# Performance work log

Hardware: AMD Instinct MI355X
Metric: run time of the kernel (lower is better)

The kernel has to match this reference:

```python
import jax, jax.numpy as jnp
import numpy as np

N_MODES = 3
NEG_SLOPE = 0.2


def setup_inputs() -> dict:
    key = jax.random.key(0)
    k1, k2, k3 = jax.random.split(key, 3)
    T, BN, C = 32, 16384, 128
    h = jax.random.normal(k1, (T, BN, C), dtype=jnp.float32)
    # FNO-style init scale 1/(in*out)
    scale = 1.0 / (C * C)
    w_real = scale * jax.random.normal(k2, (C, C, N_MODES), dtype=jnp.float32)
    w_imag = scale * jax.random.normal(k3, (C, C, N_MODES), dtype=jnp.float32)
    return {"h": h, "w_real": w_real, "w_imag": w_imag}


def reference(h, w_real, w_imag):
    T, BN, C = h.shape
    # (T, BN, C) -> (BN, C, T)
    x = jnp.transpose(h, (1, 2, 0))
    x_ft = jnp.fft.rfft(x, axis=-1)              # (BN, C, T//2+1) complex
    w = w_real + 1j * w_imag                     # (C_in, C_out, modes)
    # mix channels on the lowest n_modes frequencies
    out_low = jnp.einsum("bim,iom->bom", x_ft[..., :N_MODES], w)
    out_ft = jnp.zeros((BN, C, T // 2 + 1), dtype=x_ft.dtype)
    out_ft = out_ft.at[..., :N_MODES].set(out_low)
    y = jnp.fft.irfft(out_ft, n=T, axis=-1)      # (BN, C, T) real
    y = jnp.transpose(y, (2, 0, 1))              # back to (T, BN, C)
    return h + jnp.where(y >= 0, y, NEG_SLOPE * y)
```

## Files before the change

### kernel.cpp

```cpp
#include <hip/hip_runtime.h>
#include <hip/hip_bf16.h>


#define T 32
#define BN 16384
#define C 128
#define NBC (BN * C)

typedef __attribute__((ext_vector_type(4))) float f32x4;
typedef __attribute__((ext_vector_type(8))) short bf16x8;
typedef __attribute__((ext_vector_type(4))) unsigned short u16x4;

__constant__ float COS32[32] = {
    1.0f,           0.9807852804f,  0.9238795325f,  0.8314696123f,
    0.7071067812f,  0.5555702330f,  0.3826834324f,  0.1950903220f,
    0.0f,          -0.1950903220f, -0.3826834324f, -0.5555702330f,
   -0.7071067812f, -0.8314696123f, -0.9238795325f, -0.9807852804f,
   -1.0f,          -0.9807852804f, -0.9238795325f, -0.8314696123f,
   -0.7071067812f, -0.5555702330f, -0.3826834324f, -0.1950903220f,
    0.0f,           0.1950903220f,  0.3826834324f,  0.5555702330f,
    0.7071067812f,  0.8314696123f,  0.9238795325f,  0.9807852804f};

__constant__ float SIN32[32] = {
    0.0f,           0.1950903220f,  0.3826834324f,  0.5555702330f,
    0.7071067812f,  0.8314696123f,  0.9238795325f,  0.9807852804f,
    1.0f,           0.9807852804f,  0.9238795325f,  0.8314696123f,
    0.7071067812f,  0.5555702330f,  0.3826834324f,  0.1950903220f,
    0.0f,          -0.1950903220f, -0.3826834324f, -0.5555702330f,
   -0.7071067812f, -0.8314696123f, -0.9238795325f, -0.9807852804f,
   -1.0f,          -0.9807852804f, -0.9238795325f, -0.8314696123f,
   -0.7071067812f, -0.5555702330f, -0.3826834324f, -0.1950903220f};

__device__ __forceinline__ unsigned short f2bf(float f) {
    unsigned x = __float_as_uint(f);
    x += 0x7fffu + ((x >> 16) & 1u);
    return (unsigned short)(x >> 16);
}

__device__ __forceinline__ bf16x8 bfneg(bf16x8 a) {
    bf16x8 r;
#pragma unroll
    for (int i = 0; i < 8; ++i) r[i] = (short)(a[i] ^ (short)0x8000);
    return r;
}

__global__ __launch_bounds__(256) void k_wfrag(const float* __restrict__ wr,
                                               const float* __restrict__ wi,
                                               unsigned short* __restrict__ Wfrag) {
    int tid = blockIdx.x * 256 + threadIdx.x;
    int lane = tid & 63;
    int kk = (tid >> 6) & 3;
    int nt = (tid >> 8) & 7;
    int comp = tid >> 11;
    const float* src = (comp == 2 || comp == 4) ? wi : wr;
    int m = (comp == 0) ? 0 : ((comp <= 2) ? 1 : 2);
    int o = nt * 16 + (lane & 15);
    int kb = kk * 32 + (lane >> 4) * 8;
    unsigned short v[8];
#pragma unroll
    for (int j = 0; j < 8; ++j)
        v[j] = f2bf(src[(size_t)((kb + j) * C + o) * 3 + m]);
    u16x4* dst = (u16x4*)(Wfrag + (size_t)tid * 8);
    u16x4 lo = {v[0], v[1], v[2], v[3]};
    u16x4 hi = {v[4], v[5], v[6], v[7]};
    dst[0] = lo;
    dst[1] = hi;
}

__global__ __launch_bounds__(256) void k_xmodes(const float* __restrict__ h,
                                                unsigned short* __restrict__ Xb) {
    int idx4 = blockIdx.x * 256 + threadIdx.x;
    const f32x4* hp = (const f32x4*)h + idx4;
    f32x4 z = {0.f, 0.f, 0.f, 0.f};
    f32x4 x0 = z, x1r = z, x1i = z, x2r = z, x2i = z;
#pragma unroll
    for (int t = 0; t < T; ++t) {
        f32x4 v = hp[(size_t)t * (NBC / 4)];
        float c1 = COS32[t], s1 = SIN32[t];
        float c2 = COS32[(2 * t) & 31], s2 = SIN32[(2 * t) & 31];
        x0 += v;
        x1r += v * c1;
        x1i -= v * s1;
        x2r += v * c2;
        x2i -= v * s2;
    }
    f32x4 xs[5] = {x0, x1r, x1i, x2r, x2i};
#pragma unroll
    for (int c = 0; c < 5; ++c) {
        u16x4 o = {f2bf(xs[c][0]), f2bf(xs[c][1]), f2bf(xs[c][2]), f2bf(xs[c][3])};
        *(u16x4*)(Xb + (size_t)c * NBC + (size_t)idx4 * 4) = o;
    }
}

__global__ __launch_bounds__(256) void k_gemm(const unsigned short* __restrict__ Wfrag,
                                              const unsigned short* __restrict__ Xb,
                                              float* __restrict__ Y) {
    const int wave = threadIdx.x >> 6;
    const int lane = threadIdx.x & 63;
    const int arow = lane & 15;
    const int kgrp = lane >> 4;
    const int mbase = (blockIdx.x >> 1) * 64 + wave * 16;
    const int ntb = (blockIdx.x & 1) * 4;

    bf16x8 A[5][4];
    const unsigned short* xp = Xb + (size_t)(mbase + arow) * C + kgrp * 8;
#pragma unroll
    for (int c = 0; c < 5; ++c)
#pragma unroll
        for (int kk = 0; kk < 4; ++kk)
            A[c][kk] = *(const bf16x8*)(xp + (size_t)c * NBC + kk * 32);

    bf16x8 nA1[4], nA2[4];
#pragma unroll
    for (int kk = 0; kk < 4; ++kk) {
        nA1[kk] = bfneg(A[2][kk]);
        nA2[kk] = bfneg(A[4][kk]);
    }

    const bf16x8* wf = (const bf16x8*)Wfrag;
#pragma unroll
    for (int nto = 0; nto < 4; ++nto) {
        const int nt = ntb + nto;
        f32x4 z = {0.f, 0.f, 0.f, 0.f};
        f32x4 acc0 = z, acc1 = z, acc2 = z, acc3 = z, acc4 = z;
#pragma unroll
        for (int kk = 0; kk < 4; ++kk) {
            bf16x8 B0  = wf[(size_t)(((0 * 8 + nt) * 4 + kk) * 64) + lane];
            bf16x8 B1r = wf[(size_t)(((1 * 8 + nt) * 4 + kk) * 64) + lane];
            bf16x8 B1i = wf[(size_t)(((2 * 8 + nt) * 4 + kk) * 64) + lane];
            bf16x8 B2r = wf[(size_t)(((3 * 8 + nt) * 4 + kk) * 64) + lane];
            bf16x8 B2i = wf[(size_t)(((4 * 8 + nt) * 4 + kk) * 64) + lane];
            acc0 = __builtin_amdgcn_mfma_f32_16x16x32_bf16(A[0][kk], B0, acc0, 0, 0, 0);
            acc1 = __builtin_amdgcn_mfma_f32_16x16x32_bf16(A[1][kk], B1r, acc1, 0, 0, 0);
            acc1 = __builtin_amdgcn_mfma_f32_16x16x32_bf16(nA1[kk], B1i, acc1, 0, 0, 0);
            acc2 = __builtin_amdgcn_mfma_f32_16x16x32_bf16(A[1][kk], B1i, acc2, 0, 0, 0);
            acc2 = __builtin_amdgcn_mfma_f32_16x16x32_bf16(A[2][kk], B1r, acc2, 0, 0, 0);
            acc3 = __builtin_amdgcn_mfma_f32_16x16x32_bf16(A[3][kk], B2r, acc3, 0, 0, 0);
            acc3 = __builtin_amdgcn_mfma_f32_16x16x32_bf16(nA2[kk], B2i, acc3, 0, 0, 0);
            acc4 = __builtin_amdgcn_mfma_f32_16x16x32_bf16(A[3][kk], B2i, acc4, 0, 0, 0);
            acc4 = __builtin_amdgcn_mfma_f32_16x16x32_bf16(A[4][kk], B2r, acc4, 0, 0, 0);
        }
        const int orow = mbase + kgrp * 4;
        const int ocol = nt * 16 + arow;
#pragma unroll
        for (int r = 0; r < 4; ++r) {
            size_t off = (size_t)(orow + r) * C + ocol;
            Y[(size_t)0 * NBC + off] = acc0[r];
            Y[(size_t)1 * NBC + off] = acc1[r];
            Y[(size_t)2 * NBC + off] = acc2[r];
            Y[(size_t)3 * NBC + off] = acc3[r];
            Y[(size_t)4 * NBC + off] = acc4[r];
        }
    }
}

__global__ __launch_bounds__(256) void k_recon(const float* __restrict__ Y,
                                               const float* __restrict__ h,
                                               float* __restrict__ out) {
    int idx4 = blockIdx.x * 256 + threadIdx.x;
    const f32x4* Yp = (const f32x4*)Y;
    f32x4 y0 = Yp[(size_t)0 * (NBC / 4) + idx4] * (1.f / 32.f);
    f32x4 y1r = Yp[(size_t)1 * (NBC / 4) + idx4] * (1.f / 16.f);
    f32x4 y1i = Yp[(size_t)2 * (NBC / 4) + idx4] * (1.f / 16.f);
    f32x4 y2r = Yp[(size_t)3 * (NBC / 4) + idx4] * (1.f / 16.f);
    f32x4 y2i = Yp[(size_t)4 * (NBC / 4) + idx4] * (1.f / 16.f);
    const f32x4* hp = (const f32x4*)h + idx4;
    f32x4* op = (f32x4*)out + idx4;
#pragma unroll
    for (int t = 0; t < T; ++t) {
        float c1 = COS32[t], s1 = SIN32[t];
        float c2 = COS32[(2 * t) & 31], s2 = SIN32[(2 * t) & 31];
        f32x4 y = y0 + c1 * y1r - s1 * y1i + c2 * y2r - s2 * y2i;
        f32x4 hv = hp[(size_t)t * (NBC / 4)];
        f32x4 r;
#pragma unroll
        for (int j = 0; j < 4; ++j) {
            float v = y[j];
            r[j] = hv[j] + fmaxf(v, 0.f) + 0.2f * fminf(v, 0.f);
        }
        op[(size_t)t * (NBC / 4)] = r;
    }
}

extern "C" void kernel_launch(void* const* d_in, const int* in_sizes, int n_in,
                              void* d_out, int out_size, void* d_ws, size_t ws_size,
                              hipStream_t stream) {
    const float* h = (const float*)d_in[0];
    const float* wr = (const float*)d_in[1];
    const float* wi = (const float*)d_in[2];
    float* out = (float*)d_out;
    char* ws = (char*)d_ws;
    unsigned short* Wfrag = (unsigned short*)ws;
    unsigned short* Xb = (unsigned short*)(ws + (1u << 20));
    float* Y = (float*)(ws + (1u << 20) + (size_t)5 * NBC * 2);

    k_wfrag<<<40, 256, 0, stream>>>(wr, wi, Wfrag);
    k_xmodes<<<NBC / 1024, 256, 0, stream>>>(h, Xb);
    k_gemm<<<BN / 128, 256, 0, stream>>>(Wfrag, Xb, Y);
    k_recon<<<NBC / 1024, 256, 0, stream>>>(Y, h, out);
}
```

Measured before the change: 536.2 us.

## Fuse mode extraction, spectral GEMM and reconstruction into one kernel

Merges the forward DFT, the MFMA channel-mixing GEMM and the inverse DFT with leaky-ReLU into a single kernel. Each block handles 8 BN rows, keeps h in registers between the two passes and stages the modes and outputs in shared memory. This removes the global round trips for Xb and Y and the second read of h. It also folds the irfft scaling into the weights. The cost is that half of each 16-row MFMA tile is zero padding, so the matrix-core work doubles, and register pressure is high at 512 threads.

```diff
diff --git a/kernel.cpp b/kernel.cpp
--- a/kernel.cpp
+++ b/kernel.cpp
@@ -1,11 +1,11 @@
 #include <hip/hip_runtime.h>
-#include <hip/hip_bf16.h>
 
 
 #define T 32
 #define BN 16384
 #define C 128
 #define NBC (BN * C)
+#define NBC4 (NBC / 4)
 
 typedef __attribute__((ext_vector_type(4))) float f32x4;
 typedef __attribute__((ext_vector_type(8))) short bf16x8;
@@ -54,12 +54,13 @@
     int comp = tid >> 11;
     const float* src = (comp == 2 || comp == 4) ? wi : wr;
     int m = (comp == 0) ? 0 : ((comp <= 2) ? 1 : 2);
+    float sc = (comp == 0) ? 0.03125f : 0.0625f;
     int o = nt * 16 + (lane & 15);
     int kb = kk * 32 + (lane >> 4) * 8;
     unsigned short v[8];
 #pragma unroll
     for (int j = 0; j < 8; ++j)
-        v[j] = f2bf(src[(size_t)((kb + j) * C + o) * 3 + m]);
+        v[j] = f2bf(sc * src[(size_t)((kb + j) * C + o) * 3 + m]);
     u16x4* dst = (u16x4*)(Wfrag + (size_t)tid * 8);
     u16x4 lo = {v[0], v[1], v[2], v[3]};
     u16x4 hi = {v[4], v[5], v[6], v[7]};
@@ -67,118 +68,121 @@
     dst[1] = hi;
 }
 
-__global__ __launch_bounds__(256) void k_xmodes(const float* __restrict__ h,
-                                                unsigned short* __restrict__ Xb) {
-    int idx4 = blockIdx.x * 256 + threadIdx.x;
-    const f32x4* hp = (const f32x4*)h + idx4;
+__global__ __launch_bounds__(512) void k_main(const float* __restrict__ h,
+                                              const unsigned short* __restrict__ Wfrag,
+                                              float* __restrict__ out) {
+    __shared__ float yS[5 * 8 * C];
+    __shared__ unsigned short xS[5 * 8 * C];
+
+    const int tid = threadIdx.x;
+    const int lane = tid & 63;
+    const int wv = tid >> 6;
+    const int i4 = tid & 31;
+    const int th = (tid >> 5) & 1;
+    const int row = wv;
+    const int brow = blockIdx.x * 8;
+    const int tb = th * 16;
+
+    const f32x4* hp = (const f32x4*)h + (size_t)(brow + row) * 32 + i4;
+    f32x4 v[16];
+#pragma unroll
+    for (int tt = 0; tt < 16; ++tt) v[tt] = hp[(size_t)(tb + tt) * NBC4];
+
     f32x4 z = {0.f, 0.f, 0.f, 0.f};
     f32x4 x0 = z, x1r = z, x1i = z, x2r = z, x2i = z;
 #pragma unroll
-    for (int t = 0; t < T; ++t) {
-        f32x4 v = hp[(size_t)t * (NBC / 4)];
+    for (int tt = 0; tt < 16; ++tt) {
+        int t = tb + tt;
         float c1 = COS32[t], s1 = SIN32[t];
         float c2 = COS32[(2 * t) & 31], s2 = SIN32[(2 * t) & 31];
-        x0 += v;
-        x1r += v * c1;
-        x1i -= v * s1;
-        x2r += v * c2;
-        x2i -= v * s2;
+        f32x4 hv = v[tt];
+        x0 += hv;
+        x1r += hv * c1;
+        x1i -= hv * s1;
+        x2r += hv * c2;
+        x2i -= hv * s2;
     }
     f32x4 xs[5] = {x0, x1r, x1i, x2r, x2i};
 #pragma unroll
-    for (int c = 0; c < 5; ++c) {
-        u16x4 o = {f2bf(xs[c][0]), f2bf(xs[c][1]), f2bf(xs[c][2]), f2bf(xs[c][3])};
-        *(u16x4*)(Xb + (size_t)c * NBC + (size_t)idx4 * 4) = o;
-    }
-}
-
-__global__ __launch_bounds__(256) void k_gemm(const unsigned short* __restrict__ Wfrag,
-                                              const unsigned short* __restrict__ Xb,
-                                              float* __restrict__ Y) {
-    const int wave = threadIdx.x >> 6;
-    const int lane = threadIdx.x & 63;
-    const int arow = lane & 15;
-    const int kgrp = lane >> 4;
-    const int mbase = (blockIdx.x >> 1) * 64 + wave * 16;
-    const int ntb = (blockIdx.x & 1) * 4;
-
-    bf16x8 A[5][4];
-    const unsigned short* xp = Xb + (size_t)(mbase + arow) * C + kgrp * 8;
-#pragma unroll
     for (int c = 0; c < 5; ++c)
 #pragma unroll
-        for (int kk = 0; kk < 4; ++kk)
-            A[c][kk] = *(const bf16x8*)(xp + (size_t)c * NBC + kk * 32);
-
-    bf16x8 nA1[4], nA2[4];
-#pragma unroll
-    for (int kk = 0; kk < 4; ++kk) {
-        nA1[kk] = bfneg(A[2][kk]);
-        nA2[kk] = bfneg(A[4][kk]);
-    }
-
-    const bf16x8* wf = (const bf16x8*)Wfrag;
-#pragma unroll
-    for (int nto = 0; nto < 4; ++nto) {
-        const int nt = ntb + nto;
-        f32x4 z = {0.f, 0.f, 0.f, 0.f};
+        for (int j = 0; j < 4; ++j) xs[c][j] += __shfl_xor(xs[c][j], 32, 64);
+    if (th == 0) {
+#pragma unroll
+        for (int c = 0; c < 5; ++c) {
+            u16x4 o = {f2bf(xs[c][0]), f2bf(xs[c][1]), f2bf(xs[c][2]), f2bf(xs[c][3])};
+            *(u16x4*)&xS[(c * 8 + row) * C + i4 * 4] = o;
+        }
+    }
+    __syncthreads();
+
+    {
+        const int arow = lane & 15;
+        const int kgrp = lane >> 4;
+        const bf16x8* wf = (const bf16x8*)Wfrag;
         f32x4 acc0 = z, acc1 = z, acc2 = z, acc3 = z, acc4 = z;
 #pragma unroll
         for (int kk = 0; kk < 4; ++kk) {
-            bf16x8 B0  = wf[(size_t)(((0 * 8 + nt) * 4 + kk) * 64) + lane];
-            bf16x8 B1r = wf[(size_t)(((1 * 8 + nt) * 4 + kk) * 64) + lane];
-            bf16x8 B1i = wf[(size_t)(((2 * 8 + nt) * 4 + kk) * 64) + lane];
-            bf16x8 B2r = wf[(size_t)(((3 * 8 + nt) * 4 + kk) * 64) + lane];
-            bf16x8 B2i = wf[(size_t)(((4 * 8 + nt) * 4 + kk) * 64) + lane];
-            acc0 = __builtin_amdgcn_mfma_f32_16x16x32_bf16(A[0][kk], B0, acc0, 0, 0, 0);
-            acc1 = __builtin_amdgcn_mfma_f32_16x16x32_bf16(A[1][kk], B1r, acc1, 0, 0, 0);
-            acc1 = __builtin_amdgcn_mfma_f32_16x16x32_bf16(nA1[kk], B1i, acc1, 0, 0, 0);
-            acc2 = __builtin_amdgcn_mfma_f32_16x16x32_bf16(A[1][kk], B1i, acc2, 0, 0, 0);
-            acc2 = __builtin_amdgcn_mfma_f32_16x16x32_bf16(A[2][kk], B1r, acc2, 0, 0, 0);
-            acc3 = __builtin_amdgcn_mfma_f32_16x16x32_bf16(A[3][kk], B2r, acc3, 0, 0, 0);
-            acc3 = __builtin_amdgcn_mfma_f32_16x16x32_bf16(nA2[kk], B2i, acc3, 0, 0, 0);
-            acc4 = __builtin_amdgcn_mfma_f32_16x16x32_bf16(A[3][kk], B2i, acc4, 0, 0, 0);
-            acc4 = __builtin_amdgcn_mfma_f32_16x16x32_bf16(A[4][kk], B2r, acc4, 0, 0, 0);
+            bf16x8 A0 = {0, 0, 0, 0, 0, 0, 0, 0};
+            bf16x8 A1 = A0, A2 = A0, A3 = A0, A4 = A0;
+            if (arow < 8) {
+                const int xo = arow * C + kk * 32 + kgrp * 8;
+                A0 = *(const bf16x8*)&xS[(0 * 8) * C + xo];
+                A1 = *(const bf16x8*)&xS[(1 * 8) * C + xo];
+                A2 = *(const bf16x8*)&xS[(2 * 8) * C + xo];
+                A3 = *(const bf16x8*)&xS[(3 * 8) * C + xo];
+                A4 = *(const bf16x8*)&xS[(4 * 8) * C + xo];
+            }
+            bf16x8 nA2v = bfneg(A2);
+            bf16x8 nA4v = bfneg(A4);
+            bf16x8 B0  = wf[(size_t)(((0 * 8 + wv) * 4 + kk) * 64) + lane];
+            bf16x8 B1r = wf[(size_t)(((1 * 8 + wv) * 4 + kk) * 64) + lane];
+            bf16x8 B1i = wf[(size_t)(((2 * 8 + wv) * 4 + kk) * 64) + lane];
+            bf16x8 B2r = wf[(size_t)(((3 * 8 + wv) * 4 + kk) * 64) + lane];
+            bf16x8 B2i = wf[(size_t)(((4 * 8 + wv) * 4 + kk) * 64) + lane];
+            acc0 = __builtin_amdgcn_mfma_f32_16x16x32_bf16(A0, B0, acc0, 0, 0, 0);
+            acc1 = __builtin_amdgcn_mfma_f32_16x16x32_bf16(A1, B1r, acc1, 0, 0, 0);
+            acc1 = __builtin_amdgcn_mfma_f32_16x16x32_bf16(nA2v, B1i, acc1, 0, 0, 0);
+            acc2 = __builtin_amdgcn_mfma_f32_16x16x32_bf16(A1, B1i, acc2, 0, 0, 0);
+            acc2 = __builtin_amdgcn_mfma_f32_16x16x32_bf16(A2, B1r, acc2, 0, 0, 0);
+            acc3 = __builtin_amdgcn_mfma_f32_16x16x32_bf16(A3, B2r, acc3, 0, 0, 0);
+            acc3 = __builtin_amdgcn_mfma_f32_16x16x32_bf16(nA4v, B2i, acc3, 0, 0, 0);
+            acc4 = __builtin_amdgcn_mfma_f32_16x16x32_bf16(A3, B2i, acc4, 0, 0, 0);
+            acc4 = __builtin_amdgcn_mfma_f32_16x16x32_bf16(A4, B2r, acc4, 0, 0, 0);
         }
-        const int orow = mbase + kgrp * 4;
-        const int ocol = nt * 16 + arow;
-#pragma unroll
-        for (int r = 0; r < 4; ++r) {
-            size_t off = (size_t)(orow + r) * C + ocol;
-            Y[(size_t)0 * NBC + off] = acc0[r];
-            Y[(size_t)1 * NBC + off] = acc1[r];
-            Y[(size_t)2 * NBC + off] = acc2[r];
-            Y[(size_t)3 * NBC + off] = acc3[r];
-            Y[(size_t)4 * NBC + off] = acc4[r];
+        if (kgrp < 2) {
+            const int oc = wv * 16 + arow;
+#pragma unroll
+            for (int r = 0; r < 4; ++r) {
+                const int lrow = kgrp * 4 + r;
+                yS[(0 * 8 + lrow) * C + oc] = acc0[r];
+                yS[(1 * 8 + lrow) * C + oc] = acc1[r];
+                yS[(2 * 8 + lrow) * C + oc] = acc2[r];
+                yS[(3 * 8 + lrow) * C + oc] = acc3[r];
+                yS[(4 * 8 + lrow) * C + oc] = acc4[r];
+            }
         }
     }
-}
-
-__global__ __launch_bounds__(256) void k_recon(const float* __restrict__ Y,
-                                               const float* __restrict__ h,
-                                               float* __restrict__ out) {
-    int idx4 = blockIdx.x * 256 + threadIdx.x;
-    const f32x4* Yp = (const f32x4*)Y;
-    f32x4 y0 = Yp[(size_t)0 * (NBC / 4) + idx4] * (1.f / 32.f);
-    f32x4 y1r = Yp[(size_t)1 * (NBC / 4) + idx4] * (1.f / 16.f);
-    f32x4 y1i = Yp[(size_t)2 * (NBC / 4) + idx4] * (1.f / 16.f);
-    f32x4 y2r = Yp[(size_t)3 * (NBC / 4) + idx4] * (1.f / 16.f);
-    f32x4 y2i = Yp[(size_t)4 * (NBC / 4) + idx4] * (1.f / 16.f);
-    const f32x4* hp = (const f32x4*)h + idx4;
-    f32x4* op = (f32x4*)out + idx4;
-#pragma unroll
-    for (int t = 0; t < T; ++t) {
+    __syncthreads();
+
+    const f32x4 u0 = *(const f32x4*)&yS[(0 * 8 + row) * C + i4 * 4];
+    const f32x4 a1 = *(const f32x4*)&yS[(1 * 8 + row) * C + i4 * 4];
+    const f32x4 b1 = *(const f32x4*)&yS[(2 * 8 + row) * C + i4 * 4];
+    const f32x4 a2 = *(const f32x4*)&yS[(3 * 8 + row) * C + i4 * 4];
+    const f32x4 b2 = *(const f32x4*)&yS[(4 * 8 + row) * C + i4 * 4];
+    f32x4* op = (f32x4*)out + (size_t)(brow + row) * 32 + i4;
+#pragma unroll
+    for (int tt = 0; tt < 16; ++tt) {
+        int t = tb + tt;
         float c1 = COS32[t], s1 = SIN32[t];
         float c2 = COS32[(2 * t) & 31], s2 = SIN32[(2 * t) & 31];
-        f32x4 y = y0 + c1 * y1r - s1 * y1i + c2 * y2r - s2 * y2i;
-        f32x4 hv = hp[(size_t)t * (NBC / 4)];
+        f32x4 hv = v[tt];
+        f32x4 y = u0 + c1 * a1 - s1 * b1 + c2 * a2 - s2 * b2;
         f32x4 r;
 #pragma unroll
-        for (int j = 0; j < 4; ++j) {
-            float v = y[j];
-            r[j] = hv[j] + fmaxf(v, 0.f) + 0.2f * fminf(v, 0.f);
-        }
-        op[(size_t)t * (NBC / 4)] = r;
+        for (int j = 0; j < 4; ++j)
+            r[j] = hv[j] + fmaxf(y[j], 0.f) + 0.2f * fminf(y[j], 0.f);
+        op[(size_t)t * NBC4] = r;
     }
 }
 
@@ -189,13 +193,8 @@
     const float* wr = (const float*)d_in[1];
     const float* wi = (const float*)d_in[2];
     float* out = (float*)d_out;
-    char* ws = (char*)d_ws;
-    unsigned short* Wfrag = (unsigned short*)ws;
-    unsigned short* Xb = (unsigned short*)(ws + (1u << 20));
-    float* Y = (float*)(ws + (1u << 20) + (size_t)5 * NBC * 2);
+    unsigned short* Wfrag = (unsigned short*)d_ws;
 
     k_wfrag<<<40, 256, 0, stream>>>(wr, wi, Wfrag);
-    k_xmodes<<<NBC / 1024, 256, 0, stream>>>(h, Xb);
-    k_gemm<<<BN / 128, 256, 0, stream>>>(Wfrag, Xb, Y);
-    k_recon<<<NBC / 1024, 256, 0, stream>>>(Y, h, out);
-}
+    k_main<<<BN / 8, 512, 0, stream>>>(h, Wfrag, out);
+}
```

Measured after the change: 475.7 us. -11.3%, faster.
